# Kernel tuning notes

Hardware: AMD Instinct MI355X
Metric: run time of the kernel (lower is better)

Reference implementation:

```python
import jax, jax.numpy as jnp
import numpy as np

VOCAB, EMB, DIM_Y, DIM_Z = 30000, 100, 200, 500
DIM_H = DIM_Y + DIM_Z  # 700
B, T = 256, 256


def setup_inputs() -> dict:
    key = jax.random.key(0)
    ks = jax.random.split(key, 6)
    enc_inputs = jax.random.randint(ks[0], (B, T), 0, VOCAB, dtype=jnp.int32)
    labels = jax.random.randint(ks[1], (B,), 0, 2).astype(jnp.float32)
    embedding = jax.random.normal(ks[2], (VOCAB, EMB), dtype=jnp.float32) * 0.05
    W1 = jax.random.normal(ks[3], (1, DIM_Y), dtype=jnp.float32) * 0.1
    b1 = jnp.zeros((DIM_Y,), dtype=jnp.float32)
    Wx = jax.random.normal(ks[4], (EMB, 3 * DIM_H), dtype=jnp.float32) * (1.0 / np.sqrt(EMB))
    Wh = jax.random.normal(ks[5], (DIM_H, 3 * DIM_H), dtype=jnp.float32) * (1.0 / np.sqrt(DIM_H))
    bias = jnp.zeros((2, 3 * DIM_H), dtype=jnp.float32)  # [input_bias, recurrent_bias] (reset_after=True)
    return {"enc_inputs": enc_inputs, "labels": labels, "embedding": embedding,
            "W1": W1, "b1": b1, "Wx": Wx, "Wh": Wh, "bias": bias}


def _gru(xp, h0, Wh, b_rec):
    # xp: [T, B, 3H] precomputed input projections (+ input bias); Keras reset_after GRU.
    H = h0.shape[-1]

    def step(h, xp_t):
        rec = h @ Wh + b_rec                       # [B, 3H]
        xz, xr, xh = jnp.split(xp_t, 3, axis=-1)
        rz, rr, rh = jnp.split(rec, 3, axis=-1)
        z = jax.nn.sigmoid(xz + rz)
        r = jax.nn.sigmoid(xr + rr)
        hh = jnp.tanh(xh + r * rh)
        h_new = z * h + (1.0 - z) * hh
        return h_new, None

    h_last, _ = jax.lax.scan(step, h0, xp)
    return h_last


def reference(enc_inputs, labels, embedding, W1, b1, Wx, Wh, bias):
    x = embedding[enc_inputs]                          # [B, T, EMB]
    y0 = labels[:, None] @ W1 + b1                     # [B, dim_y]
    h0 = jnp.concatenate([y0, jnp.zeros((labels.shape[0], DIM_Z), dtype=y0.dtype)], axis=1)
    xp = jnp.einsum('bte,eh->tbh', x, Wx) + bias[0]    # [T, B, 3H]
    h_last = _gru(xp, h0, Wh, bias[1])                 # [B, dim_h]
    return h_last[:, DIM_Y:]                           # [B, dim_z]
```

## Files before the change

kernel.cpp:

```cpp
#include <hip/hip_runtime.h>


typedef unsigned short ushort_t;
typedef __bf16 bf16x8 __attribute__((ext_vector_type(8)));
typedef unsigned short ushort8 __attribute__((ext_vector_type(8)));
typedef float floatx4 __attribute__((ext_vector_type(4)));

#define NGRP   8
#define NSLC   22
#define NBLK   176
#define SB     840
#define HP     704
#define AH_ROW 1408
#define PHASE  (256 * AH_ROW)
#define FLAGW(gg, ss, ww) (256 + (gg) * 128 + (ss) * 4 + (ww))

__device__ __forceinline__ float bf2f(ushort_t u) {
    unsigned v = ((unsigned)u) << 16; float f; __builtin_memcpy(&f, &v, 4); return f;
}
__device__ __forceinline__ ushort_t f2bf(float f) {
    unsigned u; __builtin_memcpy(&u, &f, 4);
    unsigned r = u + 0x7fff + ((u >> 16) & 1);
    return (ushort_t)(r >> 16);
}
__device__ __forceinline__ bf16x8 ld8(const ushort_t* p) {
    return __builtin_bit_cast(bf16x8, *(const ushort8*)p);
}
__device__ __forceinline__ bf16x8 cvt8(floatx4 a, floatx4 b) {
    ushort8 r = {f2bf(a.x), f2bf(a.y), f2bf(a.z), f2bf(a.w),
                 f2bf(b.x), f2bf(b.y), f2bf(b.z), f2bf(b.w)};
    return __builtin_bit_cast(bf16x8, r);
}
__device__ __forceinline__ void l1_inv() {
    asm volatile("buffer_inv sc0" ::: "memory");
}
__device__ __forceinline__ void wave_drain() {
    asm volatile("s_waitcnt vmcnt(0)" ::: "memory");
}
__device__ __forceinline__ float fast_rcp(float x) {
    float r; asm("v_rcp_f32 %0, %1" : "=v"(r) : "v"(x)); return r;
}
__device__ __forceinline__ float fast_exp(float x) {
    float r; asm("v_exp_f32 %0, %1" : "=v"(r) : "v"(x * 1.44269504f)); return r;
}

__global__ void init_cnt(int* cnt) {
    for (int i = threadIdx.x; i < 1280; i += 1024) cnt[i] = 0;
}

__global__ __launch_bounds__(256, 1) void gru_main(
    const int* __restrict__ enc, const float* __restrict__ emb,
    const float* __restrict__ Wx, float* whf,
    const float* __restrict__ lab, const float* __restrict__ W1,
    const float* __restrict__ b1, const float* __restrict__ bias,
    float* __restrict__ out, int* cnt) {

    extern __shared__ ushort_t Bs[];
    const int bx = blockIdx.x;
    const int g = bx & 7, s = bx >> 3;
    const int tid = threadIdx.x;
    const int wave = tid >> 6, lane = tid & 63;
    const int rt = wave >> 1, ct = wave & 1;
    const int q = lane >> 4, m = lane & 15;

    for (int idx = tid; idx < 96 * 832; idx += 256) {
        int p = idx % 96, k = idx / 96;
        int c = s * 32 + (p & 31);
        ushort_t v = 0;
        if (c < 700) {
            int col = (p >> 5) * 700 + c;
            if (k < 100) v = f2bf(Wx[k * 2100 + col]);
            else if (k >= 128 && k < 828) v = f2bf(whf[(k - 128) * 2100 + col]);
        }
        Bs[p * SB + k] = v;
    }
    __syncthreads();

    if (tid == 0) {
        int xcc;
        asm("s_getreg_b32 %0, hwreg(HW_REG_XCC_ID)" : "=s"(xcc));
        __hip_atomic_store(cnt + 16 + bx, xcc, __ATOMIC_RELAXED, __HIP_MEMORY_SCOPE_AGENT);
        __hip_atomic_fetch_add(cnt + 8, 1, __ATOMIC_ACQ_REL, __HIP_MEMORY_SCOPE_AGENT);
        while (__hip_atomic_load(cnt + 8, __ATOMIC_ACQUIRE, __HIP_MEMORY_SCOPE_AGENT) < NBLK)
            __builtin_amdgcn_s_sleep(1);
    }
    __syncthreads();

    bool fast = true;
    {
        int myx = __hip_atomic_load(cnt + 16 + bx, __ATOMIC_RELAXED, __HIP_MEMORY_SCOPE_AGENT);
        for (int s2 = 0; s2 < NSLC; ++s2) {
            int px = __hip_atomic_load(cnt + 16 + g + 8 * s2, __ATOMIC_RELAXED, __HIP_MEMORY_SCOPE_AGENT);
            fast = fast && (px == myx);
        }
    }

    const int j = s * 32 + ct * 16 + m;
    float bzc = 0.f, brc = 0.f, b0h = 0.f, b1h = 0.f;
    if (j < 700) {
        bzc = bias[j] + bias[2100 + j];
        brc = bias[700 + j] + bias[2800 + j];
        b0h = bias[1400 + j];
        b1h = bias[3500 + j];
    }
    const int rowa = g * 32 + rt * 16 + m;

    ushort_t* Ah = (ushort_t*)whf;
    int* myflag = cnt + FLAGW(g, s, wave);
    int* pollp = (lane < 44)
               ? (cnt + FLAGW(g, lane >> 1, rt * 2 + (lane & 1)))
               : (int*)nullptr;

    float hown[4];
#pragma unroll
    for (int i = 0; i < 4; i++) {
        int rowc = g * 32 + rt * 16 + q * 4 + i;
        float v = 0.f;
        if (j < 200) v = lab[rowc] * W1[j] + b1[j];
        hown[i] = v;
        ushort_t hi = f2bf(v);
        Ah[rowc * AH_ROW + j] = hi;
        Ah[rowc * AH_ROW + HP + j] = f2bf(v - bf2f(hi));
    }
    if (fast) {
        wave_drain();
        if (lane == 0)
            __hip_atomic_store(myflag, 1, __ATOMIC_RELAXED, __HIP_MEMORY_SCOPE_AGENT);
    } else {
        if (lane == 0)
            __hip_atomic_store(myflag, 1, __ATOMIC_RELEASE, __HIP_MEMORY_SCOPE_AGENT);
        else
            __threadfence();
    }

    const ushort_t* bsz = Bs + (ct * 16 + m) * SB;
    const ushort_t* bsr = Bs + (32 + ct * 16 + m) * SB;
    const ushort_t* bsh = Bs + (64 + ct * 16 + m) * SB;

    floatx4 pf[6]; floatx4 pft;
    {
        int tok = enc[rowa * 256 + 0];
        const float* ep = emb + tok * 100;
#pragma unroll
        for (int kt = 0; kt < 3; ++kt) {
            pf[kt * 2]     = *(const floatx4*)(ep + kt * 32 + q * 8);
            pf[kt * 2 + 1] = *(const floatx4*)(ep + kt * 32 + q * 8 + 4);
        }
        pft = *(const floatx4*)(ep + 96);
    }

    for (int t = 0; t < 256; ++t) {
        const ushort_t* Asrc = Ah + (t & 1) * PHASE;
        ushort_t* Adst = Ah + ((t + 1) & 1) * PHASE;
        floatx4 accz = {0,0,0,0}, accr = {0,0,0,0}, accrh = {0,0,0,0}, accxh = {0,0,0,0};

#pragma unroll
        for (int kt = 0; kt < 3; ++kt) {
            bf16x8 a = cvt8(pf[kt * 2], pf[kt * 2 + 1]);
            int kb = kt * 32 + q * 8;
            accz  = __builtin_amdgcn_mfma_f32_16x16x32_bf16(a, ld8(bsz + kb), accz, 0, 0, 0);
            accr  = __builtin_amdgcn_mfma_f32_16x16x32_bf16(a, ld8(bsr + kb), accr, 0, 0, 0);
            accxh = __builtin_amdgcn_mfma_f32_16x16x32_bf16(a, ld8(bsh + kb), accxh, 0, 0, 0);
        }
        {
            ushort8 t8 = {0, 0, 0, 0, 0, 0, 0, 0};
            if (q == 0) {
                t8[0] = f2bf(pft.x); t8[1] = f2bf(pft.y);
                t8[2] = f2bf(pft.z); t8[3] = f2bf(pft.w);
            }
            bf16x8 a = __builtin_bit_cast(bf16x8, t8);
            int kb = 96 + q * 8;
            accz  = __builtin_amdgcn_mfma_f32_16x16x32_bf16(a, ld8(bsz + kb), accz, 0, 0, 0);
            accr  = __builtin_amdgcn_mfma_f32_16x16x32_bf16(a, ld8(bsr + kb), accr, 0, 0, 0);
            accxh = __builtin_amdgcn_mfma_f32_16x16x32_bf16(a, ld8(bsh + kb), accxh, 0, 0, 0);
        }
        {
            int tn = (t < 255) ? t + 1 : 255;
            int tok = enc[rowa * 256 + tn];
            const float* ep = emb + tok * 100;
#pragma unroll
            for (int kt = 0; kt < 3; ++kt) {
                pf[kt * 2]     = *(const floatx4*)(ep + kt * 32 + q * 8);
                pf[kt * 2 + 1] = *(const floatx4*)(ep + kt * 32 + q * 8 + 4);
            }
            pft = *(const floatx4*)(ep + 96);
        }

        if (lane < 44) {
            if (fast) {
                int spin = 0;
                while (__hip_atomic_load(pollp, __ATOMIC_RELAXED, __HIP_MEMORY_SCOPE_AGENT) < t + 1) {
                    if (++spin > 64) __builtin_amdgcn_s_sleep(1);
                }
            } else {
                while (__hip_atomic_load(pollp, __ATOMIC_ACQUIRE, __HIP_MEMORY_SCOPE_AGENT) < t + 1)
                    __builtin_amdgcn_s_sleep(1);
            }
        }
        if (fast) l1_inv();

        const ushort_t* arow = Asrc + rowa * AH_ROW + q * 8;
        bf16x8 ra[8], rb[8];
#pragma unroll
        for (int p = 0; p < 8; ++p) {
            ra[p] = ld8(arow + p * 32);
            rb[p] = ld8(arow + HP + p * 32);
        }
#pragma unroll
        for (int kt = 0; kt < 22; ++kt) {
            bf16x8 ahi = ra[kt & 7];
            bf16x8 alo = rb[kt & 7];
            if (kt + 8 < 22) {
                ra[kt & 7] = ld8(arow + (kt + 8) * 32);
                rb[kt & 7] = ld8(arow + HP + (kt + 8) * 32);
            }
            int kb = 128 + kt * 32 + q * 8;
            bf16x8 bz8 = ld8(bsz + kb), br8 = ld8(bsr + kb), bh8 = ld8(bsh + kb);
            accz  = __builtin_amdgcn_mfma_f32_16x16x32_bf16(ahi, bz8, accz, 0, 0, 0);
            accr  = __builtin_amdgcn_mfma_f32_16x16x32_bf16(ahi, br8, accr, 0, 0, 0);
            accrh = __builtin_amdgcn_mfma_f32_16x16x32_bf16(ahi, bh8, accrh, 0, 0, 0);
            accz  = __builtin_amdgcn_mfma_f32_16x16x32_bf16(alo, bz8, accz, 0, 0, 0);
            accr  = __builtin_amdgcn_mfma_f32_16x16x32_bf16(alo, br8, accr, 0, 0, 0);
            accrh = __builtin_amdgcn_mfma_f32_16x16x32_bf16(alo, bh8, accrh, 0, 0, 0);
        }

#pragma unroll
        for (int i = 0; i < 4; i++) {
            int rowc = g * 32 + rt * 16 + q * 4 + i;
            float z = fast_rcp(1.f + fast_exp(-(accz[i] + bzc)));
            float r = fast_rcp(1.f + fast_exp(-(accr[i] + brc)));
            float e2 = fast_exp(2.f * (accxh[i] + b0h + r * (accrh[i] + b1h)));
            float hh = 1.f - 2.f * fast_rcp(e2 + 1.f);
            float h = z * hown[i] + (1.f - z) * hh;
            if (j >= 700) h = 0.f;
            hown[i] = h;
            ushort_t hi = f2bf(h);
            Adst[rowc * AH_ROW + j] = hi;
            Adst[rowc * AH_ROW + HP + j] = f2bf(h - bf2f(hi));
        }

        if (fast) {
            wave_drain();
            if (lane == 0)
                __hip_atomic_store(myflag, t + 2, __ATOMIC_RELAXED, __HIP_MEMORY_SCOPE_AGENT);
        } else {
            if (lane == 0)
                __hip_atomic_store(myflag, t + 2, __ATOMIC_RELEASE, __HIP_MEMORY_SCOPE_AGENT);
            else
                __threadfence();
        }
    }

#pragma unroll
    for (int i = 0; i < 4; i++) {
        int rowc = g * 32 + rt * 16 + q * 4 + i;
        if (j >= 200 && j < 700)
            out[rowc * 500 + (j - 200)] = hown[i];
    }
}

extern "C" void kernel_launch(void* const* d_in, const int* in_sizes, int n_in,
                              void* d_out, int out_size, void* d_ws, size_t ws_size,
                              hipStream_t stream) {
    (void)in_sizes; (void)n_in; (void)out_size; (void)ws_size;
    const int*   enc  = (const int*)d_in[0];
    const float* lab  = (const float*)d_in[1];
    const float* emb  = (const float*)d_in[2];
    const float* W1   = (const float*)d_in[3];
    const float* b1   = (const float*)d_in[4];
    const float* Wx   = (const float*)d_in[5];
    float*       Wh   = (float*)d_in[6];
    const float* bias = (const float*)d_in[7];

    int*   cnt = (int*)d_ws;
    float* out = (float*)d_out;

    init_cnt<<<1, 1024, 0, stream>>>(cnt);

    hipFuncSetAttribute((const void*)gru_main,
                        hipFuncAttributeMaxDynamicSharedMemorySize, 96 * SB * 2);
    gru_main<<<NBLK, 256, 96 * SB * 2, stream>>>(enc, emb, Wx, Wh, lab, W1, b1,
                                                 bias, out, cnt);
}
```

Before: 2.083 ms.

## Poll flags via sc0 loads with agent-scope mirror fallback and earlier wait

Flags are now written twice: once with a plain sc0 global store and once as an agent-scope atomic into a mirror array. The fast spin loop polls the primary flag with sc0 loads and falls back to the mirror after a number of spins. The wait and L1 invalidate move ahead of the next-token embedding prefetch. The aim is lower latency on the inter-block step barrier, at the cost of an extra flag store per wave and a larger flag area. It also relies on sc0 visibility across CUs, which may not hold in general and is why the mirror exists.

Result: slower. 3.753 ms (+80.2%).

```diff
diff --git a/kernel.cpp b/kernel.cpp
--- a/kernel.cpp
+++ b/kernel.cpp
@@ -13,7 +13,8 @@
 #define HP     704
 #define AH_ROW 1408
 #define PHASE  (256 * AH_ROW)
-#define FLAGW(gg, ss, ww) (256 + (gg) * 128 + (ss) * 4 + (ww))
+#define FLAGW(gg, ss, ww) (256 + (gg) * 256 + (ss) * 4 + (ww))
+#define MIRROFF 128
 
 __device__ __forceinline__ float bf2f(ushort_t u) {
     unsigned v = ((unsigned)u) << 16; float f; __builtin_memcpy(&f, &v, 4); return f;
@@ -37,6 +38,16 @@
 __device__ __forceinline__ void wave_drain() {
     asm volatile("s_waitcnt vmcnt(0)" ::: "memory");
 }
+__device__ __forceinline__ void flag_store_sc0(int* p, int v) {
+    asm volatile("global_store_dword %0, %1, off sc0" :: "v"(p), "v"(v) : "memory");
+}
+__device__ __forceinline__ int flag_load_sc0(const int* p) {
+    int v;
+    asm volatile("global_load_dword %0, %1, off sc0\n\t"
+                 "s_waitcnt vmcnt(0)"
+                 : "=v"(v) : "v"(p) : "memory");
+    return v;
+}
 __device__ __forceinline__ float fast_rcp(float x) {
     float r; asm("v_rcp_f32 %0, %1" : "=v"(r) : "v"(x)); return r;
 }
@@ -45,7 +56,7 @@
 }
 
 __global__ void init_cnt(int* cnt) {
-    for (int i = threadIdx.x; i < 1280; i += 1024) cnt[i] = 0;
+    for (int i = threadIdx.x; i < 2304; i += 1024) cnt[i] = 0;
 }
 
 __global__ __launch_bounds__(256, 1) void gru_main(
@@ -107,9 +118,11 @@
 
     ushort_t* Ah = (ushort_t*)whf;
     int* myflag = cnt + FLAGW(g, s, wave);
+    int* mymirr = myflag + MIRROFF;
     int* pollp = (lane < 44)
                ? (cnt + FLAGW(g, lane >> 1, rt * 2 + (lane & 1)))
                : (int*)nullptr;
+    int* pollm = pollp ? pollp + MIRROFF : (int*)nullptr;
 
     float hown[4];
 #pragma unroll
@@ -124,8 +137,10 @@
     }
     if (fast) {
         wave_drain();
-        if (lane == 0)
-            __hip_atomic_store(myflag, 1, __ATOMIC_RELAXED, __HIP_MEMORY_SCOPE_AGENT);
+        if (lane == 0) {
+            flag_store_sc0(myflag, 1);
+            __hip_atomic_store(mymirr, 1, __ATOMIC_RELAXED, __HIP_MEMORY_SCOPE_AGENT);
+        }
     } else {
         if (lane == 0)
             __hip_atomic_store(myflag, 1, __ATOMIC_RELEASE, __HIP_MEMORY_SCOPE_AGENT);
@@ -174,6 +189,25 @@
             accr  = __builtin_amdgcn_mfma_f32_16x16x32_bf16(a, ld8(bsr + kb), accr, 0, 0, 0);
             accxh = __builtin_amdgcn_mfma_f32_16x16x32_bf16(a, ld8(bsh + kb), accxh, 0, 0, 0);
         }
+
+        if (lane < 44) {
+            if (fast) {
+                int spin = 0;
+                while (flag_load_sc0(pollp) < t + 1) {
+                    if (++spin > 64) {
+                        if (__hip_atomic_load(pollm, __ATOMIC_RELAXED,
+                                              __HIP_MEMORY_SCOPE_AGENT) >= t + 1)
+                            break;
+                        __builtin_amdgcn_s_sleep(1);
+                    }
+                }
+            } else {
+                while (__hip_atomic_load(pollp, __ATOMIC_ACQUIRE, __HIP_MEMORY_SCOPE_AGENT) < t + 1)
+                    __builtin_amdgcn_s_sleep(1);
+            }
+        }
+        if (fast) l1_inv();
+
         {
             int tn = (t < 255) ? t + 1 : 255;
             int tok = enc[rowa * 256 + tn];
@@ -185,19 +219,6 @@
             }
             pft = *(const floatx4*)(ep + 96);
         }
-
-        if (lane < 44) {
-            if (fast) {
-                int spin = 0;
-                while (__hip_atomic_load(pollp, __ATOMIC_RELAXED, __HIP_MEMORY_SCOPE_AGENT) < t + 1) {
-                    if (++spin > 64) __builtin_amdgcn_s_sleep(1);
-                }
-            } else {
-                while (__hip_atomic_load(pollp, __ATOMIC_ACQUIRE, __HIP_MEMORY_SCOPE_AGENT) < t + 1)
-                    __builtin_amdgcn_s_sleep(1);
-            }
-        }
-        if (fast) l1_inv();
 
         const ushort_t* arow = Asrc + rowa * AH_ROW + q * 8;
         bf16x8 ra[8], rb[8];
@@ -241,8 +262,10 @@
 
         if (fast) {
             wave_drain();
-            if (lane == 0)
-                __hip_atomic_store(myflag, t + 2, __ATOMIC_RELAXED, __HIP_MEMORY_SCOPE_AGENT);
+            if (lane == 0) {
+                flag_store_sc0(myflag, t + 2);
+                __hip_atomic_store(mymirr, t + 2, __ATOMIC_RELAXED, __HIP_MEMORY_SCOPE_AGENT);
+            }
         } else {
             if (lane == 0)
                 __hip_atomic_store(myflag, t + 2, __ATOMIC_RELEASE, __HIP_MEMORY_SCOPE_AGENT);
```
